# Optimization experiments

Hardware: AMD Instinct MI355X
Metric: run time of the kernel (lower is better)

Reference implementation:

```python
import jax, jax.numpy as jnp
import numpy as np

N, H, W = 128, 64, 64
CH_I, CH_H, CH_Q = 2, 150, 10
N_ACT = 8


def conv3x3(x, w):
    # x: [N,H,W,Cin], w: [3,3,Cin,Cout], 'same' padding, stride 1
    return jax.lax.conv_general_dilated(
        x, w, window_strides=(1, 1), padding='SAME',
        dimension_numbers=('NHWC', 'HWIO', 'NHWC'))


def setup_inputs() -> dict:
    key = jax.random.key(0)
    ks = jax.random.split(key, 9)
    std = 0.01
    x = jax.random.normal(ks[0], (N, H, W, CH_I), dtype=jnp.float32)
    S1 = jax.random.randint(ks[1], (N,), 0, H, dtype=jnp.int32)
    S2 = jax.random.randint(ks[2], (N,), 0, W, dtype=jnp.int32)
    w0 = std * jax.random.normal(ks[3], (3, 3, CH_I, CH_H), dtype=jnp.float32)
    b0 = jnp.zeros((CH_H,), dtype=jnp.float32)
    w_r = std * jax.random.normal(ks[4], (3, 3, CH_H, 1), dtype=jnp.float32)
    w_q = std * jax.random.normal(ks[5], (3, 3, 2, CH_Q), dtype=jnp.float32)
    w_sw = std * jax.random.normal(ks[6], (3, 3, 2, CH_Q), dtype=jnp.float32)
    w_sw2 = std * jax.random.normal(ks[7], (3, 3, 2, CH_Q), dtype=jnp.float32)
    w_dense = std * jax.random.normal(ks[8], (CH_Q, N_ACT), dtype=jnp.float32)
    return {"x": x, "S1": S1, "S2": S2, "VInum": 36,
            "w0": w0, "b0": b0, "w_r": w_r, "w_q": w_q,
            "w_sw": w_sw, "w_sw2": w_sw2, "w_dense": w_dense}


def reference(x, S1, S2, VInum, w0, b0, w_r, w_q, w_sw, w_sw2, w_dense):
    k = int(VInum)
    h = conv3x3(x, w0) + b0                      # [N,H,W,ch_h]
    r = conv3x3(h, w_r)                          # [N,H,W,1] reward map
    v = jnp.zeros_like(r)
    # first VI step uses conv2 weights
    q = conv3x3(jnp.concatenate([r, v], axis=3), w_q)
    v = jnp.max(q, axis=3, keepdims=True)
    # k-1 shared-weight value-iteration steps
    def body(v, _):
        q = conv3x3(jnp.concatenate([r, v], axis=3), w_sw)
        return jnp.max(q, axis=3, keepdims=True), None
    v, _ = jax.lax.scan(body, v, None, length=k - 1)
    # final step with second shared-weight conv
    q = conv3x3(jnp.concatenate([r, v], axis=3), w_sw2)  # [N,H,W,ch_q]
    # attention: gather Q values at state (S1,S2) per batch element
    q_out = q[jnp.arange(q.shape[0]), S1, S2]            # [N,ch_q]
    logits = q_out @ w_dense                             # [N,8]
    prob_actions = jax.nn.softmax(logits, axis=-1)
    return (logits, prob_actions, q, q_out)
```

## Files before the change

### kernel.cpp

```cpp
#include <hip/hip_runtime.h>
#include <math.h>


typedef float v2f __attribute__((ext_vector_type(2)));

static __device__ __forceinline__ v2f splat2(float s) { v2f r; r.x = s; r.y = s; return r; }
static __device__ __forceinline__ v2f pkfma(v2f w, float v, v2f a) {
#if __has_builtin(__builtin_elementwise_fma)
    return __builtin_elementwise_fma(w, splat2(v), a);
#else
    v2f r; r.x = fmaf(w.x, v, a.x); r.y = fmaf(w.y, v, a.y); return r;
#endif
}
static __device__ __forceinline__ v2f pkmax(v2f a, v2f b) {
#if __has_builtin(__builtin_elementwise_max)
    return __builtin_elementwise_max(a, b);
#else
    v2f r; r.x = fmaxf(a.x, b.x); r.y = fmaxf(a.y, b.y); return r;
#endif
}

#define XROW 69
#define VROW 67
#define VSTR (66 * VROW)

__global__ void
__attribute__((amdgpu_flat_work_group_size(512, 512)))
__attribute__((amdgpu_waves_per_eu(2, 2)))
vin_kernel(const float* __restrict__ x,
           const int* __restrict__ S1,
           const int* __restrict__ S2,
           const int* __restrict__ VInum,
           const float* __restrict__ w0,
           const float* __restrict__ b0,
           const float* __restrict__ w_r,
           const float* __restrict__ w_q,
           const float* __restrict__ w_sw,
           const float* __restrict__ w_sw2,
           const float* __restrict__ w_dense,
           float* __restrict__ out) {
    const int b = blockIdx.x;
    const int t = threadIdx.x;

    __shared__ float xs0[68 * XROW];
    __shared__ float xs1[68 * XROW];
    __shared__ float rs[66 * VROW];
    __shared__ float vpool[2 * VSTR];
    __shared__ float wtA[1620];
    __shared__ float Pp[450];
    __shared__ float Bt[90];
    __shared__ float Bv[9];
    __shared__ float W5c[459];
    __shared__ v2f   swv2[45];
    __shared__ float qsel[10];

    for (int i = t; i < 68 * XROW; i += 512) { xs0[i] = 0.f; xs1[i] = 0.f; }
    for (int i = t; i < 66 * VROW; i += 512) rs[i] = 0.f;
    for (int i = t; i < 2 * VSTR; i += 512) vpool[i] = 0.f;
    if (t < 450) Pp[t] = 0.f;
    if (t < 45) {
        int d = t / 5, ap = t - d * 5;
        v2f w; w.x = w_sw[d * 20 + 10 + 2 * ap]; w.y = w_sw[d * 20 + 10 + 2 * ap + 1];
        swv2[t] = w;
    }
    __syncthreads();

    const int row = t >> 3;
    const int cb  = (t & 7) << 3;

    {
        const float* xb = x + (size_t)b * 64 * 64 * 2;
        const float4* xp = (const float4*)(xb + (row * 64 + cb) * 2);
        #pragma unroll
        for (int g = 0; g < 4; ++g) {
            float4 v4 = xp[g];
            int px = cb + g * 2;
            xs0[(row + 2) * XROW + px + 2] = v4.x;
            xs1[(row + 2) * XROW + px + 2] = v4.y;
            xs0[(row + 2) * XROW + px + 3] = v4.z;
            xs1[(row + 2) * XROW + px + 3] = v4.w;
        }
    }
    for (int idx = t; idx < 1620; idx += 512) {
        int entry = idx / 10, ch = idx - entry * 10;
        int d = entry / 18, rem = entry % 18;
        int uu = rem >> 1, ci = rem & 1;
        int c0 = ch * 15;
        const float* wr = w_r + d * 150;
        const float* wp = w0 + (uu * 2 + ci) * 150;
        float s = 0.f;
        for (int c = c0; c < c0 + 15; ++c) s += wr[c] * wp[c];
        wtA[idx] = s;
    }
    if (t < 90) {
        int d = t / 10, ch = t - d * 10, c0 = ch * 15;
        float s = 0.f;
        for (int c = c0; c < c0 + 15; ++c) s += w_r[d * 150 + c] * b0[c];
        Bt[t] = s;
    }
    __syncthreads();
    if (t < 162) {
        float s = 0.f;
        #pragma unroll
        for (int i = 0; i < 10; ++i) s += wtA[t * 10 + i];
        int d = t / 18, rem = t % 18;
        int uu = rem >> 1, ci = rem & 1;
        int dy = d / 3 - 1, dx = d % 3 - 1;
        int uy = uu / 3 - 1, ux = uu % 3 - 1;
        int eidx = (dy + uy + 2) * 5 + (dx + ux + 2);
        Pp[d * 50 + eidx * 2 + ci] = s;
    } else if (t >= 256 && t < 265) {
        int d = t - 256;
        float s = 0.f;
        #pragma unroll
        for (int i = 0; i < 10; ++i) s += Bt[d * 10 + i];
        Bv[d] = s;
    }
    __syncthreads();
    if (t < 459) {
        int cls = t / 51, j = t - cls * 51;
        int cy = cls / 3, cx = cls % 3;
        float s = 0.f;
        #pragma unroll
        for (int d = 0; d < 9; ++d) {
            int dy = d / 3 - 1, dx = d % 3 - 1;
            bool ok = (cy == 0 || (cy == 1 ? dy >= 0 : dy <= 0)) &&
                      (cx == 0 || (cx == 1 ? dx >= 0 : dx <= 0));
            if (ok) s += (j < 50) ? Pp[d * 50 + j] : Bv[d];
        }
        W5c[t] = s;
    }
    __syncthreads();

    {
        int cy = (row == 0) ? 1 : (row == 63) ? 2 : 0;
        #pragma unroll
        for (int p = 0; p < 8; ++p) {
            int xx = cb + p;
            int cx = (xx == 0) ? 1 : (xx == 63) ? 2 : 0;
            const float* Wp = &W5c[(cy * 3 + cx) * 51];
            float acc = Wp[50];
            #pragma unroll
            for (int e = 0; e < 25; ++e) {
                int xi = (row + e / 5) * XROW + (xx + e % 5);
                acc = fmaf(xs0[xi], Wp[e * 2], acc);
                acc = fmaf(xs1[xi], Wp[e * 2 + 1], acc);
            }
            rs[(row + 1) * VROW + (xx + 1)] = acc;
        }
    }
    __syncthreads();

    const int K = VInum[0];

    v2f Rsw2[8][5];
    {
        float rwin[3][10];
        #pragma unroll
        for (int i = 0; i < 3; ++i) {
            const float* rp = &rs[(row + i) * VROW + cb];
            #pragma unroll
            for (int j = 0; j < 10; ++j) rwin[i][j] = rp[j];
        }
        float vmax[8];
        #pragma unroll
        for (int a = 0; a < 10; ++a) {
            #pragma unroll
            for (int p = 0; p < 8; ++p) {
                float accR = 0.f, accQ = 0.f;
                #pragma unroll
                for (int d = 0; d < 9; ++d) {
                    float rv = rwin[d / 3][p + d % 3];
                    accR = fmaf(w_sw[d * 20 + a], rv, accR);
                    accQ = fmaf(w_q[d * 20 + a],  rv, accQ);
                }
                if (a & 1) Rsw2[p][a >> 1].y = accR; else Rsw2[p][a >> 1].x = accR;
                vmax[p] = (a == 0) ? accQ : fmaxf(vmax[p], accQ);
            }
        }
        #pragma unroll
        for (int p = 0; p < 8; ++p)
            vpool[0 * VSTR + (row + 1) * VROW + (cb + p + 1)] = vmax[p];
    }
    __syncthreads();

    v2f wreg[45];
    #pragma unroll
    for (int i = 0; i < 45; ++i) wreg[i] = swv2[i];

    int cur = 0;
    for (int it = 0; it < K - 1; ++it) {
        const float* vb = &vpool[cur * VSTR + row * VROW + cb];
        float vwin[3][10];
        #pragma unroll
        for (int i = 0; i < 3; ++i)
            #pragma unroll
            for (int j = 0; j < 10; ++j) vwin[i][j] = vb[i * VROW + j];
        int nxt = cur ^ 1;
        v2f vmax2[8];
        #pragma unroll
        for (int ap = 0; ap < 5; ++ap) {
            v2f acc2[8];
            #pragma unroll
            for (int d = 0; d < 9; ++d) {
                v2f w2 = wreg[d * 5 + ap];
                #pragma unroll
                for (int p = 0; p < 8; ++p) {
                    float vv = vwin[d / 3][p + d % 3];
                    acc2[p] = (d == 0) ? pkfma(w2, vv, Rsw2[p][ap])
                                       : pkfma(w2, vv, acc2[p]);
                }
            }
            #pragma unroll
            for (int p = 0; p < 8; ++p)
                vmax2[p] = (ap == 0) ? acc2[p] : pkmax(vmax2[p], acc2[p]);
        }
        #pragma unroll
        for (int p = 0; p < 8; ++p)
            vpool[nxt * VSTR + (row + 1) * VROW + (cb + p + 1)] =
                fmaxf(vmax2[p].x, vmax2[p].y);
        cur = nxt;
        __syncthreads();
    }

    const int s1 = S1[b], s2 = S2[b];
    {
        float rwin[3][10], vwin[3][10];
        #pragma unroll
        for (int i = 0; i < 3; ++i) {
            const float* rp = &rs[(row + i) * VROW + cb];
            const float* vb = &vpool[cur * VSTR + (row + i) * VROW + cb];
            #pragma unroll
            for (int j = 0; j < 10; ++j) { rwin[i][j] = rp[j]; vwin[i][j] = vb[j]; }
        }
        float qv[8][10];
        #pragma unroll
        for (int a = 0; a < 10; ++a) {
            #pragma unroll
            for (int p = 0; p < 8; ++p) {
                float acc = 0.f;
                #pragma unroll
                for (int d = 0; d < 9; ++d) {
                    acc = fmaf(w_sw2[d * 20 + a],      rwin[d / 3][p + d % 3], acc);
                    acc = fmaf(w_sw2[d * 20 + 10 + a], vwin[d / 3][p + d % 3], acc);
                }
                qv[p][a] = acc;
            }
        }
        {
            float4* qp4 = (float4*)(out + 2048 + ((size_t)((b * 64 + row) * 64 + cb)) * 10);
            #pragma unroll
            for (int g = 0; g < 20; ++g)
                qp4[g] = make_float4(qv[(g * 4) / 10][(g * 4) % 10],
                                     qv[(g * 4 + 1) / 10][(g * 4 + 1) % 10],
                                     qv[(g * 4 + 2) / 10][(g * 4 + 2) % 10],
                                     qv[(g * 4 + 3) / 10][(g * 4 + 3) % 10]);
        }
        if (row == s1) {
            #pragma unroll
            for (int p = 0; p < 8; ++p)
                if (s2 == cb + p) {
                    #pragma unroll
                    for (int a = 0; a < 10; ++a) qsel[a] = qv[p][a];
                }
        }
    }
    __syncthreads();

    if (t == 0) {
        float logits[8];
        float m = -1e30f;
        #pragma unroll
        for (int j = 0; j < 8; ++j) {
            float s = 0.f;
            #pragma unroll
            for (int a = 0; a < 10; ++a) s += qsel[a] * w_dense[a * 8 + j];
            logits[j] = s;
            m = fmaxf(m, s);
        }
        float sum = 0.f;
        float e[8];
        #pragma unroll
        for (int j = 0; j < 8; ++j) { e[j] = expf(logits[j] - m); sum += e[j]; }
        float inv = 1.f / sum;
        #pragma unroll
        for (int j = 0; j < 8; ++j) {
            out[b * 8 + j] = logits[j];
            out[1024 + b * 8 + j] = e[j] * inv;
        }
    }
    if (t < 10) out[5244928 + b * 10 + t] = qsel[t];
}

extern "C" void kernel_launch(void* const* d_in, const int* in_sizes, int n_in,
                              void* d_out, int out_size, void* d_ws, size_t ws_size,
                              hipStream_t stream) {
    const float* x      = (const float*)d_in[0];
    const int*   S1     = (const int*)d_in[1];
    const int*   S2     = (const int*)d_in[2];
    const int*   VInum  = (const int*)d_in[3];
    const float* w0     = (const float*)d_in[4];
    const float* b0     = (const float*)d_in[5];
    const float* w_r    = (const float*)d_in[6];
    const float* w_q    = (const float*)d_in[7];
    const float* w_sw   = (const float*)d_in[8];
    const float* w_sw2  = (const float*)d_in[9];
    const float* w_dense= (const float*)d_in[10];
    float* out = (float*)d_out;

    vin_kernel<<<128, 512, 0, stream>>>(x, S1, S2, VInum, w0, b0, w_r, w_q,
                                        w_sw, w_sw2, w_dense, out);
}
```

Measured before the change: 182.5 us.

## Split each image across two blocks with global-memory halo exchange per VI step

Each batch image is now handled by two workgroups, each owning 32 rows. The launch grows from 128 to 256 blocks so all CUs on the MI355X get work. After every value-iteration step the boundary row is published to global workspace with release/acquire flags, and each block spin-waits for its peer's halo row. The centre row of the value window is also kept in registers instead of being reloaded from LDS. The cost is cross-block spin synchronisation each iteration and a memset of the flags. Correctness relies on both peer blocks being co-resident, and the blockIdx remapping is meant to place peers on the same XCD.

```diff
diff --git a/kernel.cpp b/kernel.cpp
--- a/kernel.cpp
+++ b/kernel.cpp
@@ -22,7 +22,10 @@
 
 #define XROW 69
 #define VROW 67
-#define VSTR (66 * VROW)
+#define XS_ROWS 38
+#define RS_ROWS 34
+#define VP_ROWS 34
+#define VSTR (VP_ROWS * VROW)
 
 __global__ void
 __attribute__((amdgpu_flat_work_group_size(512, 512)))
@@ -38,13 +41,24 @@
            const float* __restrict__ w_sw,
            const float* __restrict__ w_sw2,
            const float* __restrict__ w_dense,
-           float* __restrict__ out) {
-    const int b = blockIdx.x;
+           float* __restrict__ out,
+           void* __restrict__ ws) {
+    const int g = blockIdx.x;
     const int t = threadIdx.x;
-
-    __shared__ float xs0[68 * XROW];
-    __shared__ float xs1[68 * XROW];
-    __shared__ float rs[66 * VROW];
+    const int xcd  = g & 7;
+    const int slot = g >> 3;
+    const int b    = xcd * 16 + (slot >> 1);
+    const int h    = slot & 1;
+    const int s    = h << 5;
+
+    int*   F    = (int*)ws;
+    float* Hbuf = (float*)ws + 256;
+    const int selfIdx = b * 2 + h;
+    const int peerIdx = b * 2 + (h ^ 1);
+
+    __shared__ float xs0[XS_ROWS * XROW];
+    __shared__ float xs1[XS_ROWS * XROW];
+    __shared__ float rs[RS_ROWS * VROW];
     __shared__ float vpool[2 * VSTR];
     __shared__ float wtA[1620];
     __shared__ float Pp[450];
@@ -54,8 +68,8 @@
     __shared__ v2f   swv2[45];
     __shared__ float qsel[10];
 
-    for (int i = t; i < 68 * XROW; i += 512) { xs0[i] = 0.f; xs1[i] = 0.f; }
-    for (int i = t; i < 66 * VROW; i += 512) rs[i] = 0.f;
+    for (int i = t; i < XS_ROWS * XROW; i += 512) { xs0[i] = 0.f; xs1[i] = 0.f; }
+    for (int i = t; i < RS_ROWS * VROW; i += 512) rs[i] = 0.f;
     for (int i = t; i < 2 * VSTR; i += 512) vpool[i] = 0.f;
     if (t < 450) Pp[t] = 0.f;
     if (t < 45) {
@@ -65,21 +79,14 @@
     }
     __syncthreads();
 
-    const int row = t >> 3;
-    const int cb  = (t & 7) << 3;
-
-    {
-        const float* xb = x + (size_t)b * 64 * 64 * 2;
-        const float4* xp = (const float4*)(xb + (row * 64 + cb) * 2);
-        #pragma unroll
-        for (int g = 0; g < 4; ++g) {
-            float4 v4 = xp[g];
-            int px = cb + g * 2;
-            xs0[(row + 2) * XROW + px + 2] = v4.x;
-            xs1[(row + 2) * XROW + px + 2] = v4.y;
-            xs0[(row + 2) * XROW + px + 3] = v4.z;
-            xs1[(row + 2) * XROW + px + 3] = v4.w;
-        }
+    for (int i = t; i < XS_ROWS * 32; i += 512) {
+        int xl = i >> 5, grp = i & 31;
+        int gx = s - 3 + xl;
+        if (gx < 0 || gx > 63) continue;
+        float4 v4 = *(const float4*)(x + ((size_t)(b * 64 + gx) * 64 + grp * 2) * 2);
+        int px = grp * 2;
+        xs0[xl * XROW + px + 2] = v4.x; xs1[xl * XROW + px + 2] = v4.y;
+        xs0[xl * XROW + px + 3] = v4.z; xs1[xl * XROW + px + 3] = v4.w;
     }
     for (int idx = t; idx < 1620; idx += 512) {
         int entry = idx / 10, ch = idx - entry * 10;
@@ -88,85 +95,91 @@
         int c0 = ch * 15;
         const float* wr = w_r + d * 150;
         const float* wp = w0 + (uu * 2 + ci) * 150;
-        float s = 0.f;
-        for (int c = c0; c < c0 + 15; ++c) s += wr[c] * wp[c];
-        wtA[idx] = s;
+        float ssum = 0.f;
+        for (int c = c0; c < c0 + 15; ++c) ssum += wr[c] * wp[c];
+        wtA[idx] = ssum;
     }
     if (t < 90) {
         int d = t / 10, ch = t - d * 10, c0 = ch * 15;
-        float s = 0.f;
-        for (int c = c0; c < c0 + 15; ++c) s += w_r[d * 150 + c] * b0[c];
-        Bt[t] = s;
+        float ssum = 0.f;
+        for (int c = c0; c < c0 + 15; ++c) ssum += w_r[d * 150 + c] * b0[c];
+        Bt[t] = ssum;
     }
     __syncthreads();
     if (t < 162) {
-        float s = 0.f;
-        #pragma unroll
-        for (int i = 0; i < 10; ++i) s += wtA[t * 10 + i];
+        float ssum = 0.f;
+        #pragma unroll
+        for (int i = 0; i < 10; ++i) ssum += wtA[t * 10 + i];
         int d = t / 18, rem = t % 18;
         int uu = rem >> 1, ci = rem & 1;
         int dy = d / 3 - 1, dx = d % 3 - 1;
         int uy = uu / 3 - 1, ux = uu % 3 - 1;
         int eidx = (dy + uy + 2) * 5 + (dx + ux + 2);
-        Pp[d * 50 + eidx * 2 + ci] = s;
+        Pp[d * 50 + eidx * 2 + ci] = ssum;
     } else if (t >= 256 && t < 265) {
         int d = t - 256;
-        float s = 0.f;
-        #pragma unroll
-        for (int i = 0; i < 10; ++i) s += Bt[d * 10 + i];
-        Bv[d] = s;
+        float ssum = 0.f;
+        #pragma unroll
+        for (int i = 0; i < 10; ++i) ssum += Bt[d * 10 + i];
+        Bv[d] = ssum;
     }
     __syncthreads();
     if (t < 459) {
         int cls = t / 51, j = t - cls * 51;
         int cy = cls / 3, cx = cls % 3;
-        float s = 0.f;
+        float ssum = 0.f;
         #pragma unroll
         for (int d = 0; d < 9; ++d) {
             int dy = d / 3 - 1, dx = d % 3 - 1;
             bool ok = (cy == 0 || (cy == 1 ? dy >= 0 : dy <= 0)) &&
                       (cx == 0 || (cx == 1 ? dx >= 0 : dx <= 0));
-            if (ok) s += (j < 50) ? Pp[d * 50 + j] : Bv[d];
-        }
-        W5c[t] = s;
-    }
-    __syncthreads();
-
+            if (ok) ssum += (j < 50) ? Pp[d * 50 + j] : Bv[d];
+        }
+        W5c[t] = ssum;
+    }
+    __syncthreads();
+
+    for (int i = t; i < RS_ROWS * 64; i += 512) {
+        int ri = i >> 6;
+        int c  = i & 63;
+        int gy = s + ri - 1;
+        if (gy < 0 || gy > 63) continue;
+        int cy = (gy == 0) ? 1 : (gy == 63) ? 2 : 0;
+        int cx = (c == 0) ? 1 : (c == 63) ? 2 : 0;
+        const float* Wp = &W5c[(cy * 3 + cx) * 51];
+        float acc = Wp[50];
+        #pragma unroll
+        for (int e = 0; e < 25; ++e) {
+            int xi = (ri + e / 5) * XROW + (c + e % 5);
+            acc = fmaf(xs0[xi], Wp[e * 2], acc);
+            acc = fmaf(xs1[xi], Wp[e * 2 + 1], acc);
+        }
+        rs[ri * VROW + (c + 1)] = acc;
+    }
+    __syncthreads();
+
+    const int K = VInum[0];
+    const int rl = t >> 4;
+    const int cb = (t & 15) << 2;
+    const int edgeRl  = (h == 0) ? 31 : 0;
+    const int haloRow = (h == 0) ? 33 : 0;
+    const bool isEdge = (rl == edgeRl);
+
+    v2f Rsw2[4][5];
+    float vprev[4];
     {
-        int cy = (row == 0) ? 1 : (row == 63) ? 2 : 0;
-        #pragma unroll
-        for (int p = 0; p < 8; ++p) {
-            int xx = cb + p;
-            int cx = (xx == 0) ? 1 : (xx == 63) ? 2 : 0;
-            const float* Wp = &W5c[(cy * 3 + cx) * 51];
-            float acc = Wp[50];
-            #pragma unroll
-            for (int e = 0; e < 25; ++e) {
-                int xi = (row + e / 5) * XROW + (xx + e % 5);
-                acc = fmaf(xs0[xi], Wp[e * 2], acc);
-                acc = fmaf(xs1[xi], Wp[e * 2 + 1], acc);
-            }
-            rs[(row + 1) * VROW + (xx + 1)] = acc;
-        }
-    }
-    __syncthreads();
-
-    const int K = VInum[0];
-
-    v2f Rsw2[8][5];
-    {
-        float rwin[3][10];
+        float rwin[3][6];
         #pragma unroll
         for (int i = 0; i < 3; ++i) {
-            const float* rp = &rs[(row + i) * VROW + cb];
-            #pragma unroll
-            for (int j = 0; j < 10; ++j) rwin[i][j] = rp[j];
-        }
-        float vmax[8];
+            const float* rp = &rs[(rl + i) * VROW + cb];
+            #pragma unroll
+            for (int j = 0; j < 6; ++j) rwin[i][j] = rp[j];
+        }
+        float vmax[4];
         #pragma unroll
         for (int a = 0; a < 10; ++a) {
             #pragma unroll
-            for (int p = 0; p < 8; ++p) {
+            for (int p = 0; p < 4; ++p) {
                 float accR = 0.f, accQ = 0.f;
                 #pragma unroll
                 for (int d = 0; d < 9; ++d) {
@@ -178,9 +191,26 @@
                 vmax[p] = (a == 0) ? accQ : fmaxf(vmax[p], accQ);
             }
         }
-        #pragma unroll
-        for (int p = 0; p < 8; ++p)
-            vpool[0 * VSTR + (row + 1) * VROW + (cb + p + 1)] = vmax[p];
+        if (isEdge) {
+            float* dst = Hbuf + (selfIdx * 2 + 1) * 64 + cb;
+            #pragma unroll
+            for (int p = 0; p < 4; ++p)
+                __hip_atomic_store(&dst[p], vmax[p], __ATOMIC_RELAXED, __HIP_MEMORY_SCOPE_AGENT);
+            if ((t & 15) == 0)
+                __hip_atomic_store(&F[selfIdx], 1, __ATOMIC_RELEASE, __HIP_MEMORY_SCOPE_AGENT);
+        }
+        #pragma unroll
+        for (int p = 0; p < 4; ++p) {
+            vpool[0 * VSTR + (rl + 1) * VROW + (cb + p + 1)] = vmax[p];
+            vprev[p] = vmax[p];
+        }
+    }
+    if (t < 64) {
+        while (__hip_atomic_load(&F[peerIdx], __ATOMIC_ACQUIRE, __HIP_MEMORY_SCOPE_AGENT) < 1)
+            __builtin_amdgcn_s_sleep(2);
+        float hv = __hip_atomic_load(&Hbuf[(peerIdx * 2 + 1) * 64 + t],
+                                     __ATOMIC_RELAXED, __HIP_MEMORY_SCOPE_AGENT);
+        vpool[0 * VSTR + haloRow * VROW + (t + 1)] = hv;
     }
     __syncthreads();
 
@@ -189,55 +219,90 @@
     for (int i = 0; i < 45; ++i) wreg[i] = swv2[i];
 
     int cur = 0;
-    for (int it = 0; it < K - 1; ++it) {
-        const float* vb = &vpool[cur * VSTR + row * VROW + cb];
-        float vwin[3][10];
-        #pragma unroll
-        for (int i = 0; i < 3; ++i)
-            #pragma unroll
-            for (int j = 0; j < 10; ++j) vwin[i][j] = vb[i * VROW + j];
+    for (int k = 2; k <= K; ++k) {
+        const float* vb = &vpool[cur * VSTR + rl * VROW + cb];
+        float v0[6], v2[6];
+        #pragma unroll
+        for (int j = 0; j < 6; ++j) v0[j] = vb[j];
+        #pragma unroll
+        for (int j = 0; j < 6; ++j) v2[j] = vb[2 * VROW + j];
+        float eL = vb[VROW], eR = vb[VROW + 5];
+        float v1[6];
+        v1[0] = eL; v1[5] = eR;
+        #pragma unroll
+        for (int j = 0; j < 4; ++j) v1[j + 1] = vprev[j];
+
         int nxt = cur ^ 1;
-        v2f vmax2[8];
+        v2f vmax2[4];
         #pragma unroll
         for (int ap = 0; ap < 5; ++ap) {
-            v2f acc2[8];
+            v2f acc[4];
             #pragma unroll
             for (int d = 0; d < 9; ++d) {
                 v2f w2 = wreg[d * 5 + ap];
+                const float* vr = (d < 3) ? v0 : (d < 6) ? v1 : v2;
                 #pragma unroll
-                for (int p = 0; p < 8; ++p) {
-                    float vv = vwin[d / 3][p + d % 3];
-                    acc2[p] = (d == 0) ? pkfma(w2, vv, Rsw2[p][ap])
-                                       : pkfma(w2, vv, acc2[p]);
+                for (int p = 0; p < 4; ++p) {
+                    float vv = vr[p + d % 3];
+                    acc[p] = (d == 0) ? pkfma(w2, vv, Rsw2[p][ap])
+                                      : pkfma(w2, vv, acc[p]);
                 }
             }
             #pragma unroll
-            for (int p = 0; p < 8; ++p)
-                vmax2[p] = (ap == 0) ? acc2[p] : pkmax(vmax2[p], acc2[p]);
-        }
-        #pragma unroll
-        for (int p = 0; p < 8; ++p)
-            vpool[nxt * VSTR + (row + 1) * VROW + (cb + p + 1)] =
-                fmaxf(vmax2[p].x, vmax2[p].y);
+            for (int p = 0; p < 4; ++p)
+                vmax2[p] = (ap == 0) ? acc[p] : pkmax(vmax2[p], acc[p]);
+        }
+        float vnew[4];
+        #pragma unroll
+        for (int p = 0; p < 4; ++p) vnew[p] = fmaxf(vmax2[p].x, vmax2[p].y);
+
+        if (isEdge) {
+            float* dst = Hbuf + (selfIdx * 2 + (k & 1)) * 64 + cb;
+            #pragma unroll
+            for (int p = 0; p < 4; ++p)
+                __hip_atomic_store(&dst[p], vnew[p], __ATOMIC_RELAXED, __HIP_MEMORY_SCOPE_AGENT);
+            if ((t & 15) == 0)
+                __hip_atomic_store(&F[selfIdx], k, __ATOMIC_RELEASE, __HIP_MEMORY_SCOPE_AGENT);
+        }
+        float* vw = &vpool[nxt * VSTR + (rl + 1) * VROW + cb + 1];
+        #pragma unroll
+        for (int p = 0; p < 4; ++p) { vw[p] = vnew[p]; vprev[p] = vnew[p]; }
+
+        if (t < 64) {
+            while (__hip_atomic_load(&F[peerIdx], __ATOMIC_ACQUIRE, __HIP_MEMORY_SCOPE_AGENT) < k)
+                __builtin_amdgcn_s_sleep(2);
+            float hv = __hip_atomic_load(&Hbuf[(peerIdx * 2 + (k & 1)) * 64 + t],
+                                         __ATOMIC_RELAXED, __HIP_MEMORY_SCOPE_AGENT);
+            vpool[nxt * VSTR + haloRow * VROW + (t + 1)] = hv;
+        }
+        __syncthreads();
         cur = nxt;
-        __syncthreads();
     }
 
     const int s1 = S1[b], s2 = S2[b];
+    const int gy = s + rl;
     {
-        float rwin[3][10], vwin[3][10];
+        float rwin[3][6], vwin[3][6];
         #pragma unroll
         for (int i = 0; i < 3; ++i) {
-            const float* rp = &rs[(row + i) * VROW + cb];
-            const float* vb = &vpool[cur * VSTR + (row + i) * VROW + cb];
-            #pragma unroll
-            for (int j = 0; j < 10; ++j) { rwin[i][j] = rp[j]; vwin[i][j] = vb[j]; }
-        }
-        float qv[8][10];
+            const float* rp = &rs[(rl + i) * VROW + cb];
+            #pragma unroll
+            for (int j = 0; j < 6; ++j) rwin[i][j] = rp[j];
+        }
+        const float* vb = &vpool[cur * VSTR + rl * VROW + cb];
+        #pragma unroll
+        for (int j = 0; j < 6; ++j) vwin[0][j] = vb[j];
+        #pragma unroll
+        for (int j = 0; j < 6; ++j) vwin[2][j] = vb[2 * VROW + j];
+        vwin[1][0] = vb[VROW]; vwin[1][5] = vb[VROW + 5];
+        #pragma unroll
+        for (int j = 0; j < 4; ++j) vwin[1][j + 1] = vprev[j];
+
+        float qv[4][10];
         #pragma unroll
         for (int a = 0; a < 10; ++a) {
             #pragma unroll
-            for (int p = 0; p < 8; ++p) {
+            for (int p = 0; p < 4; ++p) {
                 float acc = 0.f;
                 #pragma unroll
                 for (int d = 0; d < 9; ++d) {
@@ -248,17 +313,17 @@
             }
         }
         {
-            float4* qp4 = (float4*)(out + 2048 + ((size_t)((b * 64 + row) * 64 + cb)) * 10);
-            #pragma unroll
-            for (int g = 0; g < 20; ++g)
-                qp4[g] = make_float4(qv[(g * 4) / 10][(g * 4) % 10],
-                                     qv[(g * 4 + 1) / 10][(g * 4 + 1) % 10],
-                                     qv[(g * 4 + 2) / 10][(g * 4 + 2) % 10],
-                                     qv[(g * 4 + 3) / 10][(g * 4 + 3) % 10]);
-        }
-        if (row == s1) {
-            #pragma unroll
-            for (int p = 0; p < 8; ++p)
+            float4* qp4 = (float4*)(out + 2048 + ((size_t)((b * 64 + gy) * 64 + cb)) * 10);
+            #pragma unroll
+            for (int gq = 0; gq < 10; ++gq)
+                qp4[gq] = make_float4(qv[(gq * 4) / 10][(gq * 4) % 10],
+                                      qv[(gq * 4 + 1) / 10][(gq * 4 + 1) % 10],
+                                      qv[(gq * 4 + 2) / 10][(gq * 4 + 2) % 10],
+                                      qv[(gq * 4 + 3) / 10][(gq * 4 + 3) % 10]);
+        }
+        if ((s1 >> 5) == h && rl == (s1 & 31)) {
+            #pragma unroll
+            for (int p = 0; p < 4; ++p)
                 if (s2 == cb + p) {
                     #pragma unroll
                     for (int a = 0; a < 10; ++a) qsel[a] = qv[p][a];
@@ -267,29 +332,31 @@
     }
     __syncthreads();
 
-    if (t == 0) {
-        float logits[8];
-        float m = -1e30f;
-        #pragma unroll
-        for (int j = 0; j < 8; ++j) {
-            float s = 0.f;
-            #pragma unroll
-            for (int a = 0; a < 10; ++a) s += qsel[a] * w_dense[a * 8 + j];
-            logits[j] = s;
-            m = fmaxf(m, s);
-        }
-        float sum = 0.f;
-        float e[8];
-        #pragma unroll
-        for (int j = 0; j < 8; ++j) { e[j] = expf(logits[j] - m); sum += e[j]; }
-        float inv = 1.f / sum;
-        #pragma unroll
-        for (int j = 0; j < 8; ++j) {
-            out[b * 8 + j] = logits[j];
-            out[1024 + b * 8 + j] = e[j] * inv;
-        }
-    }
-    if (t < 10) out[5244928 + b * 10 + t] = qsel[t];
+    if ((s1 >> 5) == h) {
+        if (t == 0) {
+            float logits[8];
+            float m = -1e30f;
+            #pragma unroll
+            for (int j = 0; j < 8; ++j) {
+                float ssum = 0.f;
+                #pragma unroll
+                for (int a = 0; a < 10; ++a) ssum += qsel[a] * w_dense[a * 8 + j];
+                logits[j] = ssum;
+                m = fmaxf(m, ssum);
+            }
+            float sum = 0.f;
+            float e[8];
+            #pragma unroll
+            for (int j = 0; j < 8; ++j) { e[j] = expf(logits[j] - m); sum += e[j]; }
+            float inv = 1.f / sum;
+            #pragma unroll
+            for (int j = 0; j < 8; ++j) {
+                out[b * 8 + j] = logits[j];
+                out[1024 + b * 8 + j] = e[j] * inv;
+            }
+        }
+        if (t < 10) out[5244928 + b * 10 + t] = qsel[t];
+    }
 }
 
 extern "C" void kernel_launch(void* const* d_in, const int* in_sizes, int n_in,
@@ -308,6 +375,7 @@
     const float* w_dense= (const float*)d_in[10];
     float* out = (float*)d_out;
 
-    vin_kernel<<<128, 512, 0, stream>>>(x, S1, S2, VInum, w0, b0, w_r, w_q,
-                                        w_sw, w_sw2, w_dense, out);
+    hipMemsetAsync(d_ws, 0, 256 * sizeof(int), stream);
+    vin_kernel<<<256, 512, 0, stream>>>(x, S1, S2, VInum, w0, b0, w_r, w_q,
+                                        w_sw, w_sw2, w_dense, out, d_ws);
 }
```

New measurement: 449.0 us. 146% more time.
